# Kernel tuning notes

Measured on AMD Instinct MI355X. Metric: run time of the kernel, lower is better.

The kernel has to match this reference:

```python
import jax, jax.numpy as jnp
import numpy as np

# Winograd F(2x2, 3x3) transform matrices (G matches the module's self.G)
_BT = np.array([[1, 0, -1, 0], [0, 1, 1, 0], [0, -1, 1, 0], [0, 1, 0, -1]], dtype=np.float32)
_G = np.array([[1, 0, 0], [0.5, 0.5, 0.5], [0.5, -0.5, 0.5], [0, 0, 1]], dtype=np.float32)
_AT = np.array([[1, 1, 1, 0], [0, 1, -1, -1]], dtype=np.float32)

PAD = 1  # module padding


def setup_inputs() -> dict:
    key = jax.random.key(0)
    k1, k2, k3 = jax.random.split(key, 3)
    x = jax.random.normal(k1, (16, 128, 112, 112), dtype=jnp.float32)
    weight = jax.random.normal(k2, (128, 128, 3, 3), dtype=jnp.float32) * 0.05
    bias = jax.random.normal(k3, (128,), dtype=jnp.float32) * 0.05
    return {"x": x, "weight": weight, "bias": bias}


def reference(x, weight, bias):
    # Winograd F(2x2,3x3) convolution, stride=1, padding=PAD.
    N, C, H, W = x.shape
    O = weight.shape[0]
    oh = H + 2 * PAD - 2
    ow = W + 2 * PAD - 2
    nth = -(-oh // 2)  # number of 2x2 output tiles along H
    ntw = -(-ow // 2)
    Hp = 2 * nth + 2  # padded size so every tile has a full 4x4 input patch
    Wp = 2 * ntw + 2
    xp = jnp.pad(x, ((0, 0), (0, 0), (PAD, Hp - H - PAD), (PAD, Wp - W - PAD)))

    # Gather overlapping 4x4 input tiles with stride 2 -> (N, C, nth, ntw, 4, 4)
    ih = (jnp.arange(nth) * 2)[:, None] + jnp.arange(4)[None, :]
    iw = (jnp.arange(ntw) * 2)[:, None] + jnp.arange(4)[None, :]
    tiles = xp[:, :, ih[:, None, :, None], iw[None, :, None, :]]

    Bt = jnp.asarray(_BT)
    G = jnp.asarray(_G)
    At = jnp.asarray(_AT)

    # Input transform: V = B^T d B   -> (N, C, nth, ntw, 4, 4)
    V = jnp.einsum('ij,nctujk,lk->nctuil', Bt, tiles, Bt)
    # Filter transform: U = G g G^T  -> (O, C, 4, 4)
    U = jnp.einsum('ij,ocjk,lk->ocil', G, weight, G)
    # Elementwise multiply in Winograd domain, contract over input channels
    M = jnp.einsum('ocij,nctuij->notuij', U, V)
    # Output transform: y = A^T M A  -> (N, O, nth, ntw, 2, 2)
    Yt = jnp.einsum('ai,notuij,bj->notuab', At, M, At)

    # Reassemble tiles into the output image and crop to (oh, ow)
    Y = Yt.transpose(0, 1, 2, 4, 3, 5).reshape(N, O, 2 * nth, 2 * ntw)[:, :, :oh, :ow]
    return Y + bias[None, :, None, None]
```

## Files before the change

### kernel.cpp

```cpp
#include <hip/hip_runtime.h>
#include <hip/hip_bf16.h>

typedef __bf16 bf16x8 __attribute__((ext_vector_type(8)));
typedef float f32x4 __attribute__((ext_vector_type(4)));

#define HH 112
#define WW 112
#define CIN 128
#define COUT 128
#define HP 114
#define WP 114

#define RRV 10
#define RCV 18

__global__ void wino_prep_weights(const float* __restrict__ w,
                                  __hip_bfloat16* __restrict__ wb) {
    int t = blockIdx.x * 256 + threadIdx.x;
    if (t >= 9 * COUT * CIN) return;
    int c = t & (CIN - 1);
    int o = (t >> 7) & (COUT - 1);
    int r = t >> 14;
    wb[t] = __float2bfloat16(w[(o * CIN + c) * 9 + r]);
}

__global__ void pad_borders(__hip_bfloat16* __restrict__ xt) {
    int q = blockIdx.x * 256 + threadIdx.x;
    int n = blockIdx.y;
    if (q >= 452 * 16) return;
    int chunk = q & 15;
    int cell = q >> 4;
    int hp, wp;
    if (cell < 114)      { hp = 0;          wp = cell; }
    else if (cell < 228) { hp = 113;        wp = cell - 114; }
    else if (cell < 340) { hp = cell - 227; wp = 0; }
    else                 { hp = cell - 339; wp = 113; }
    bf16x8 z = {};
    *reinterpret_cast<bf16x8*>(xt + ((size_t)(n * HP + hp) * WP + wp) * CIN + chunk * 8) = z;
}

__global__ __launch_bounds__(256) void transpose_pad(
        const float* __restrict__ x, __hip_bfloat16* __restrict__ xt) {
    const int wl = threadIdx.x & 15;
    const int cg = threadIdx.x >> 4;
    const int w = blockIdx.x * 16 + wl;
    const int h = blockIdx.y;
    const int n = blockIdx.z;
    const float* src = x + (((size_t)(n * CIN + cg * 8) * HH + h) * WW) + w;
    float v[8];
#pragma unroll
    for (int j = 0; j < 8; ++j) v[j] = src[(size_t)j * HH * WW];
    union { bf16x8 v8; __hip_bfloat16 e[8]; } o;
#pragma unroll
    for (int j = 0; j < 8; ++j) o.e[j] = __float2bfloat16(v[j]);
    *reinterpret_cast<bf16x8*>(
        xt + ((size_t)(n * HP + h + 1) * WP + (w + 1)) * CIN + cg * 8) = o.v8;
}

__device__ __forceinline__ void gload_lds16(const __hip_bfloat16* g, __hip_bfloat16* l) {
    __builtin_amdgcn_global_load_lds(
        (const __attribute__((address_space(1))) unsigned int*)g,
        (__attribute__((address_space(3))) unsigned int*)l, 16, 0, 0);
}

__global__ __launch_bounds__(256, 3) void conv3x3_mfma(
        const __hip_bfloat16* __restrict__ xt, const __hip_bfloat16* __restrict__ wb,
        const float* __restrict__ bias, float* __restrict__ out) {
    __shared__ __align__(16) __hip_bfloat16 xs[2][RRV * RCV * 32];

    const int ox0 = blockIdx.x * 16, oy0 = blockIdx.y * 8;
    const int n = blockIdx.z;
    const int tid = threadIdx.x;
    const int lane = tid & 63;
    const int wv = tid >> 6;
    const int wo = wv >> 1;
    const int wp = wv & 1;
    const int l15 = lane & 15;
    const int lg = lane >> 4;

    f32x4 acc[4][4];
#pragma unroll
    for (int i = 0; i < 4; ++i)
#pragma unroll
        for (int j = 0; j < 4; ++j) acc[i][j] = (f32x4){0.f, 0.f, 0.f, 0.f};

    const __hip_bfloat16* gb0 = xt + (((size_t)n * HP + oy0) * WP + ox0) * CIN;

    int s_row[3], s_col[3], s_sub[3], s_act[3];
#pragma unroll
    for (int it = 0; it < 3; ++it) {
        int q = tid + it * 256;
        s_act[it] = (q < RRV * RCV * 4);
        int cell = q >> 2;
        int row = cell / RCV;
        s_row[it] = row;
        s_col[it] = cell - row * RCV;
        s_sub[it] = q & 3;
    }

    auto stage = [&](int buf, int cc) {
        const __hip_bfloat16* gb = gb0 + cc * 32;
#pragma unroll
        for (int it = 0; it < 3; ++it) {
            int q = tid + it * 256;
            if (s_act[it])
                gload_lds16(gb + ((size_t)(s_row[it] * WP + s_col[it])) * CIN + s_sub[it] * 8,
                            &xs[buf][q * 8]);
        }
    };

    stage(0, 0);
    __syncthreads();

#pragma unroll 1
    for (int cc = 0; cc < 4; ++cc) {
        if (cc < 3) stage((cc + 1) & 1, cc + 1);
        const int buf = cc & 1;
        const int cbase = cc * 32;
#pragma unroll
        for (int off = 0; off < 9; ++off) {
            const int dy = (off * 11) >> 5;
            const int dx = off - dy * 3;
            bf16x8 af[4];
            const __hip_bfloat16* wbase =
                wb + ((size_t)(off * COUT) + wo * 64 + l15) * CIN + cbase + lg * 8;
#pragma unroll
            for (int os = 0; os < 4; ++os)
                af[os] = *reinterpret_cast<const bf16x8*>(wbase + os * 16 * CIN);
            bf16x8 bfr[4];
#pragma unroll
            for (int ps = 0; ps < 4; ++ps) {
                int row = wp * 4 + ps + dy;
                int col = l15 + dx;
                bfr[ps] = *reinterpret_cast<const bf16x8*>(
                    &xs[buf][((row * RCV + col) * 32) + lg * 8]);
            }
#pragma unroll
            for (int os = 0; os < 4; ++os)
#pragma unroll
                for (int ps = 0; ps < 4; ++ps)
                    acc[os][ps] = __builtin_amdgcn_mfma_f32_16x16x32_bf16(
                        af[os], bfr[ps], acc[os][ps], 0, 0, 0);
        }
        __syncthreads();
    }

#pragma unroll
    for (int os = 0; os < 4; ++os) {
#pragma unroll
        for (int r = 0; r < 4; ++r) {
            int o = wo * 64 + os * 16 + lg * 4 + r;
            float bv = bias[o];
            float* obase = out + (((size_t)(n * COUT + o) * HH + oy0 + wp * 4) * WW) + ox0 + l15;
#pragma unroll
            for (int ps = 0; ps < 4; ++ps)
                obase[ps * WW] = acc[os][ps][r] + bv;
        }
    }
}

extern "C" void kernel_launch(void* const* d_in, const int* in_sizes, int n_in,
                              void* d_out, int out_size, void* d_ws, size_t ws_size,
                              hipStream_t stream) {
    const float* x = (const float*)d_in[0];
    const float* w = (const float*)d_in[1];
    const float* bias = (const float*)d_in[2];
    float* out = (float*)d_out;

    __hip_bfloat16* xt = (__hip_bfloat16*)d_ws;
    __hip_bfloat16* wb = (__hip_bfloat16*)((char*)d_ws + 53231616);

    hipLaunchKernelGGL(wino_prep_weights, dim3(576), dim3(256), 0, stream, w, wb);
    hipLaunchKernelGGL(pad_borders, dim3((452 * 16 + 255) / 256, 16), dim3(256), 0, stream, xt);
    hipLaunchKernelGGL(transpose_pad, dim3(7, 112, 16), dim3(256), 0, stream, x, xt);
    hipLaunchKernelGGL(conv3x3_mfma, dim3(7, 14, 16), dim3(256), 0, stream,
                       xt, wb, bias, out);
}
```

Baseline: 335.6 us.

## Reuse LDS input rows across filter rows, swizzle LDS, vectorize transpose and stores

The conv loop is reorganized by filter column so that each LDS input row fragment is loaded once and reused across up to three filter rows. This cuts LDS reads from 36 to 18 per channel chunk, at the cost of holding 12 weight fragments in registers. An XOR swizzle on the LDS layout is meant to reduce bank conflicts. MFMA operands are swapped so the output can be written as 16-byte vector stores, and the transpose kernel is rewritten to use vectorized f32x4 reads with packed bf16 pair writes, which adds register pressure.

```diff
diff --git a/kernel.cpp b/kernel.cpp
--- a/kernel.cpp
+++ b/kernel.cpp
@@ -13,6 +13,9 @@
 
 #define RRV 10
 #define RCV 18
+#define NQ (RRV * RCV * 4)
+
+__device__ __forceinline__ int swz(int Q) { return Q ^ ((Q >> 3) & 7); }
 
 __global__ void wino_prep_weights(const float* __restrict__ w,
                                   __hip_bfloat16* __restrict__ wb) {
@@ -41,20 +44,30 @@
 
 __global__ __launch_bounds__(256) void transpose_pad(
         const float* __restrict__ x, __hip_bfloat16* __restrict__ xt) {
-    const int wl = threadIdx.x & 15;
-    const int cg = threadIdx.x >> 4;
-    const int w = blockIdx.x * 16 + wl;
-    const int h = blockIdx.y;
-    const int n = blockIdx.z;
-    const float* src = x + (((size_t)(n * CIN + cg * 8) * HH + h) * WW) + w;
-    float v[8];
+    const int t = threadIdx.x;
+    const int cp = t & 63;
+    const int ws = (t >> 6) & 1;
+    const int hh = t >> 7;
+    const int h = blockIdx.x * 2 + hh;
+    const int n = blockIdx.y;
+
+    const float* s0 = x + (((size_t)(n * CIN + cp * 2) * HH + h) * WW) + ws * 56;
+    const float* s1 = s0 + (size_t)HH * WW;
+    f32x4 a[14], b[14];
 #pragma unroll
-    for (int j = 0; j < 8; ++j) v[j] = src[(size_t)j * HH * WW];
-    union { bf16x8 v8; __hip_bfloat16 e[8]; } o;
+    for (int k = 0; k < 14; ++k) a[k] = *reinterpret_cast<const f32x4*>(s0 + k * 4);
 #pragma unroll
-    for (int j = 0; j < 8; ++j) o.e[j] = __float2bfloat16(v[j]);
-    *reinterpret_cast<bf16x8*>(
-        xt + ((size_t)(n * HP + h + 1) * WP + (w + 1)) * CIN + cg * 8) = o.v8;
+    for (int k = 0; k < 14; ++k) b[k] = *reinterpret_cast<const f32x4*>(s1 + k * 4);
+
+    unsigned* dst = reinterpret_cast<unsigned*>(xt) +
+                    ((size_t)(n * HP + h + 1) * WP + (ws * 56 + 1)) * (CIN / 2) + cp;
+#pragma unroll
+    for (int k = 0; k < 56; ++k) {
+        union { __hip_bfloat16 e[2]; unsigned u; } p;
+        p.e[0] = __float2bfloat16(a[k >> 2][k & 3]);
+        p.e[1] = __float2bfloat16(b[k >> 2][k & 3]);
+        dst[(size_t)k * (CIN / 2)] = p.u;
+    }
 }
 
 __device__ __forceinline__ void gload_lds16(const __hip_bfloat16* g, __hip_bfloat16* l) {
@@ -66,7 +79,7 @@
 __global__ __launch_bounds__(256, 3) void conv3x3_mfma(
         const __hip_bfloat16* __restrict__ xt, const __hip_bfloat16* __restrict__ wb,
         const float* __restrict__ bias, float* __restrict__ out) {
-    __shared__ __align__(16) __hip_bfloat16 xs[2][RRV * RCV * 32];
+    __shared__ __align__(16) __hip_bfloat16 xs[2][NQ * 8];
 
     const int ox0 = blockIdx.x * 16, oy0 = blockIdx.y * 8;
     const int n = blockIdx.z;
@@ -86,28 +99,31 @@
 
     const __hip_bfloat16* gb0 = xt + (((size_t)n * HP + oy0) * WP + ox0) * CIN;
 
-    int s_row[3], s_col[3], s_sub[3], s_act[3];
+    int g_off[3];
 #pragma unroll
     for (int it = 0; it < 3; ++it) {
         int q = tid + it * 256;
-        s_act[it] = (q < RRV * RCV * 4);
-        int cell = q >> 2;
-        int row = cell / RCV;
-        s_row[it] = row;
-        s_col[it] = cell - row * RCV;
-        s_sub[it] = q & 3;
+        if (q < NQ) {
+            int Q = swz(q);
+            int cell = Q >> 2;
+            int row = cell / RCV;
+            int col = cell - row * RCV;
+            g_off[it] = (row * WP + col) * CIN + (Q & 3) * 8;
+        } else {
+            g_off[it] = 0;
+        }
     }
 
     auto stage = [&](int buf, int cc) {
-        const __hip_bfloat16* gb = gb0 + cc * 32;
 #pragma unroll
         for (int it = 0; it < 3; ++it) {
             int q = tid + it * 256;
-            if (s_act[it])
-                gload_lds16(gb + ((size_t)(s_row[it] * WP + s_col[it])) * CIN + s_sub[it] * 8,
-                            &xs[buf][q * 8]);
+            if (q < NQ)
+                gload_lds16(gb0 + cc * 32 + g_off[it], &xs[buf][q * 8]);
         }
     };
+
+    const int qbase = ((wp * 4) * RCV + l15) * 4 + lg;
 
     stage(0, 0);
     __syncthreads();
@@ -115,46 +131,48 @@
 #pragma unroll 1
     for (int cc = 0; cc < 4; ++cc) {
         if (cc < 3) stage((cc + 1) & 1, cc + 1);
-        const int buf = cc & 1;
-        const int cbase = cc * 32;
+        const __hip_bfloat16* xb = xs[cc & 1];
+        const int cb = cc * 32;
 #pragma unroll
-        for (int off = 0; off < 9; ++off) {
-            const int dy = (off * 11) >> 5;
-            const int dx = off - dy * 3;
-            bf16x8 af[4];
-            const __hip_bfloat16* wbase =
-                wb + ((size_t)(off * COUT) + wo * 64 + l15) * CIN + cbase + lg * 8;
+        for (int dx = 0; dx < 3; ++dx) {
+            bf16x8 Wf[3][4];
 #pragma unroll
-            for (int os = 0; os < 4; ++os)
-                af[os] = *reinterpret_cast<const bf16x8*>(wbase + os * 16 * CIN);
-            bf16x8 bfr[4];
+            for (int dy = 0; dy < 3; ++dy)
 #pragma unroll
-            for (int ps = 0; ps < 4; ++ps) {
-                int row = wp * 4 + ps + dy;
-                int col = l15 + dx;
-                bfr[ps] = *reinterpret_cast<const bf16x8*>(
-                    &xs[buf][((row * RCV + col) * 32) + lg * 8]);
+                for (int os = 0; os < 4; ++os)
+                    Wf[dy][os] = *reinterpret_cast<const bf16x8*>(
+                        wb + ((size_t)((dy * 3 + dx) * COUT) + wo * 64 + os * 16 + l15) * CIN
+                           + cb + lg * 8);
+#pragma unroll
+            for (int r = 0; r < 6; ++r) {
+                int Q = qbase + r * (RCV * 4) + dx * 4;
+                bf16x8 F = *reinterpret_cast<const bf16x8*>(&xb[swz(Q) * 8]);
+#pragma unroll
+                for (int dy = 0; dy < 3; ++dy) {
+                    int ps = r - dy;
+                    if (ps >= 0 && ps < 4) {
+#pragma unroll
+                        for (int os = 0; os < 4; ++os)
+                            acc[os][ps] = __builtin_amdgcn_mfma_f32_16x16x32_bf16(
+                                F, Wf[dy][os], acc[os][ps], 0, 0, 0);
+                    }
+                }
             }
-#pragma unroll
-            for (int os = 0; os < 4; ++os)
-#pragma unroll
-                for (int ps = 0; ps < 4; ++ps)
-                    acc[os][ps] = __builtin_amdgcn_mfma_f32_16x16x32_bf16(
-                        af[os], bfr[ps], acc[os][ps], 0, 0, 0);
         }
         __syncthreads();
     }
 
 #pragma unroll
     for (int os = 0; os < 4; ++os) {
+        int o = wo * 64 + os * 16 + l15;
+        float bv = bias[o];
 #pragma unroll
-        for (int r = 0; r < 4; ++r) {
-            int o = wo * 64 + os * 16 + lg * 4 + r;
-            float bv = bias[o];
-            float* obase = out + (((size_t)(n * COUT + o) * HH + oy0 + wp * 4) * WW) + ox0 + l15;
+        for (int ps = 0; ps < 4; ++ps) {
+            f32x4 v;
 #pragma unroll
-            for (int ps = 0; ps < 4; ++ps)
-                obase[ps * WW] = acc[os][ps][r] + bv;
+            for (int e = 0; e < 4; ++e) v[e] = acc[os][ps][e] + bv;
+            *reinterpret_cast<f32x4*>(
+                out + (((size_t)(n * COUT + o) * HH + oy0 + wp * 4 + ps) * WW) + ox0 + lg * 4) = v;
         }
     }
 }
@@ -172,7 +190,7 @@
 
     hipLaunchKernelGGL(wino_prep_weights, dim3(576), dim3(256), 0, stream, w, wb);
     hipLaunchKernelGGL(pad_borders, dim3((452 * 16 + 255) / 256, 16), dim3(256), 0, stream, xt);
-    hipLaunchKernelGGL(transpose_pad, dim3(7, 112, 16), dim3(256), 0, stream, x, xt);
+    hipLaunchKernelGGL(transpose_pad, dim3(56, 16), dim3(256), 0, stream, x, xt);
     hipLaunchKernelGGL(conv3x3_mfma, dim3(7, 14, 16), dim3(256), 0, stream,
                        xt, wb, bias, out);
 }
```

Result: no change. 338.0 us (+0.7%).
